# Optimization experiments

Hardware: AMD Instinct MI355X
Metric: run time of the kernel (lower is better)

Reference implementation:

```python
import jax, jax.numpy as jnp
import numpy as np

NGRID, NLAYER = 8192, 24
NPERIODS, NOBS, NC = 50, 4096, 200
SIGMA = 1.0
VREF = 3.0          # reference crustal Vs (km/s) for depth-sensitivity scale
RAYLEIGH_FACTOR = 0.92


def setup_inputs() -> dict:
    key = jax.random.key(0)
    k1, k2, k3 = jax.random.split(key, 3)
    # S-wave velocity model, 2.0-4.0 km/s, flattened as in log_prob(Vs_flat)
    Vs_flat = (2.0 + 2.0 * jax.random.uniform(k1, (NGRID, NLAYER))).reshape(-1).astype(jnp.float32)
    # Ray-path averaging matrix: nonnegative, rows sum to 1 (slowness average)
    A = jax.random.uniform(k2, (NOBS, NGRID), dtype=jnp.float32)
    A = A / A.sum(axis=1, keepdims=True)
    # Beamforming energy spectra per observation pair: (Nobs, Nperiods, Nc)
    energy = jax.random.uniform(k3, (NOBS, NPERIODS, NC), dtype=jnp.float32)
    # Monotone phase-velocity axis per observation: (Nobs, Nc)
    c_axis = jnp.zeros((NOBS, NC), jnp.float32) + jnp.linspace(1.5, 5.0, NC, dtype=jnp.float32)
    thick = jnp.full((NLAYER,), 2.0, jnp.float32)          # 2 km layers
    periods = jnp.linspace(1.0, 60.0, NPERIODS, dtype=jnp.float32)
    return {"Vs_flat": Vs_flat, "A": A, "energy": energy, "c_axis": c_axis,
            "thick": thick, "periods": periods}


def _dispersion_all_cells(Vs, thick, periods):
    # Differentiable surrogate for the batched surf96 forward across all grid cells.
    # Vs: (G, L), thick: (L,), periods: (P,)  ->  c_true: (G, P)
    z = jnp.cumsum(thick) - 0.5 * thick                      # layer-center depths (L,)
    depth_scale = VREF * periods / 3.0                       # ~ sensing depth per period (P,)
    w = jnp.exp(-z[None, :] / depth_scale[:, None]) * thick[None, :]  # (P, L)
    w = w / w.sum(axis=1, keepdims=True)
    return RAYLEIGH_FACTOR * jnp.einsum('pl,gl->gp', w, Vs)  # (G, P)


def reference(Vs_flat, A, energy, c_axis, thick, periods):
    Vs = Vs_flat.reshape(NGRID, NLAYER)
    c_true = _dispersion_all_cells(Vs, thick, periods)       # (Ngrid, Nperiods)
    # _apply_A: slowness averaging along ray paths
    s_pred = A @ (1.0 / c_true)                              # (Nobs, Nperiods)
    c_pred = 1.0 / s_pred
    # _interp1d_torch, vectorized over all (obs, period) pairs
    idx = jax.vmap(jnp.searchsorted)(c_axis, c_pred)         # (Nobs, Nperiods)
    idx = jnp.clip(idx, 1, NC - 1)
    c0 = jnp.take_along_axis(c_axis, idx - 1, axis=1)
    c1 = jnp.take_along_axis(c_axis, idx, axis=1)
    e0 = jnp.take_along_axis(energy, (idx - 1)[:, :, None], axis=2)[..., 0]
    e1 = jnp.take_along_axis(energy, idx[:, :, None], axis=2)[..., 0]
    w = (c_pred - c0) / (c1 - c0 + 1e-12)
    e_interp = e0 + w * (e1 - e0)
    e_max = energy.max(axis=-1)                              # (Nobs, Nperiods)
    log_like = -jnp.sum(e_max - e_interp) / (SIGMA ** 2)
    return log_like
```

## Files before the change

kernel.cpp:

```cpp
#include <hip/hip_runtime.h>

#define NGRID 8192
#define NLAYER 24
#define NPERIODS 50
#define NOBS 4096
#define NC 200
#define PP 64
#define NSPLIT 16
#define WPB 4
#define GC (NGRID / (NSPLIT * WPB))
#define KG 32
#define ASTR 36
#define NBINS 1024
#define OTILE 64
#define VREF 3.0f

__global__ __launch_bounds__(256) void k1_rpad(const float* __restrict__ Vs,
                                               const float* __restrict__ thick,
                                               const float* __restrict__ periods,
                                               float* __restrict__ r_pad,
                                               float* __restrict__ bins) {
    __shared__ float w_sh[NLAYER][NPERIODS];
    __shared__ float z_sh[NLAYER];
    int tid = threadIdx.x;
    if (blockIdx.x == 0) {
        for (int i = tid; i < NBINS; i += 256) bins[i] = 0.f;
    }
    if (tid < NLAYER) {
        float c = 0.f;
        for (int i = 0; i <= tid; ++i) c += thick[i];
        z_sh[tid] = c - 0.5f * thick[tid];
    }
    __syncthreads();
    if (tid < NPERIODS) {
        float ds = (VREF / 3.0f) * periods[tid];
        float tmp[NLAYER];
        float s = 0.f;
        #pragma unroll
        for (int l = 0; l < NLAYER; ++l) {
            float v = expf(-z_sh[l] / ds) * thick[l];
            tmp[l] = v; s += v;
        }
        float inv = 1.f / s;
        #pragma unroll
        for (int l = 0; l < NLAYER; ++l) w_sh[l][tid] = tmp[l] * inv;
    }
    __syncthreads();
    int idx = blockIdx.x * 256 + tid;
    int g = idx >> 6, p = idx & 63;
    float r = 0.f;
    if (p < NPERIODS) {
        const float4* vp = (const float4*)(Vs + (size_t)g * NLAYER);
        float s = 0.f;
        #pragma unroll
        for (int q = 0; q < NLAYER / 4; ++q) {
            float4 t = vp[q];
            s = fmaf(w_sh[4*q+0][p], t.x, s);
            s = fmaf(w_sh[4*q+1][p], t.y, s);
            s = fmaf(w_sh[4*q+2][p], t.z, s);
            s = fmaf(w_sh[4*q+3][p], t.w, s);
        }
        r = 1.0f / (0.92f * s);
    }
    r_pad[idx] = r;
}

__global__ __launch_bounds__(256) void k2_gemm(const float* __restrict__ A,
                                               const float* __restrict__ r_pad,
                                               float* __restrict__ partial) {
    __shared__ float lds[WPB * OTILE * ASTR];
    int tid  = threadIdx.x;
    int lane = tid & 63;
    int wv   = __builtin_amdgcn_readfirstlane(tid >> 6);
    int o_base = blockIdx.x * OTILE;
    int split  = blockIdx.y;
    float* Aw = lds + wv * (OTILE * ASTR);

    float acc[NPERIODS];
    #pragma unroll
    for (int p = 0; p < NPERIODS; ++p) acc[p] = 0.f;

    int g_wave = (split * WPB + wv) * GC;

    #pragma unroll 1
    for (int kt = 0; kt < GC / KG; ++kt) {
        int g0 = g_wave + kt * KG;
        #pragma unroll
        for (int s = 0; s < 8; ++s) {
            int f   = s * 64 + lane;
            int row = f >> 3;
            int c4  = (f & 7) * 4;
            float4 t = *(const float4*)(A + (size_t)(o_base + row) * NGRID + g0 + c4);
            *(float4*)(Aw + row * ASTR + c4) = t;
        }
        #pragma unroll 1
        for (int gg = 0; gg < KG; gg += 4) {
            float4 a4 = *(const float4*)(Aw + lane * ASTR + gg);
            const float* rr = r_pad + (size_t)(g0 + gg) * PP;
            #pragma unroll
            for (int j = 0; j < 4; ++j) {
                float aj = (j == 0) ? a4.x : (j == 1) ? a4.y : (j == 2) ? a4.z : a4.w;
                const float* rj = rr + j * PP;
                #pragma unroll
                for (int p = 0; p < NPERIODS; ++p) acc[p] = fmaf(aj, rj[p], acc[p]);
            }
        }
    }

    float* outp = partial + (size_t)split * (NOBS * NPERIODS) + (size_t)o_base * NPERIODS;
    #pragma unroll 1
    for (int h = 0; h < 4; ++h) {
        __syncthreads();
        float* rw = lds + wv * (OTILE * 17);
        #pragma unroll
        for (int q = 0; q < 16; ++q) {
            int p = h * 16 + q;
            rw[lane * 17 + q] = (p < NPERIODS) ? acc[p] : 0.f;
        }
        __syncthreads();
        for (int e = tid; e < OTILE * 16; e += 256) {
            int oo = e >> 4, q = e & 15;
            int p  = h * 16 + q;
            if (p < NPERIODS) {
                float v = 0.f;
                #pragma unroll
                for (int w2 = 0; w2 < WPB; ++w2) v += lds[w2 * (OTILE * 17) + oo * 17 + q];
                outp[oo * NPERIODS + p] = v;
            }
        }
    }
}

__global__ __launch_bounds__(256) void k2b_reduce(const float* __restrict__ partial,
                                                  float* __restrict__ cpred) {
    int idx = blockIdx.x * 256 + threadIdx.x;
    int o = idx >> 6, p = idx & 63;
    float v = 0.f;
    if (p < NPERIODS) {
        float s = 0.f;
        #pragma unroll
        for (int sp = 0; sp < NSPLIT; ++sp)
            s += partial[(size_t)sp * (NOBS * NPERIODS) + (size_t)o * NPERIODS + p];
        v = 1.0f / s;
    }
    cpred[idx] = v;
}

__global__ __launch_bounds__(256) void k3_main(const float* __restrict__ energy,
                                               const float* __restrict__ c_axis,
                                               const float* __restrict__ cpred,
                                               float* __restrict__ bins) {
    __shared__ float csh[NC];
    __shared__ float red[4];
    int tid  = threadIdx.x;
    int lane = tid & 63;
    int wv   = tid >> 6;
    int o    = blockIdx.x;

    if (tid < NC) csh[tid] = c_axis[(size_t)o * NC + tid];
    __syncthreads();

    bool act = lane < NC / 4;
    float4 ca = act ? *(const float4*)(csh + 4 * lane) : make_float4(9e30f, 9e30f, 9e30f, 9e30f);
    const float* ebase = energy + (size_t)o * NPERIODS * NC;
    float local = 0.f;

    for (int p0 = wv; p0 < NPERIODS; p0 += 8) {
        int p1 = p0 + 4;
        bool has1 = p1 < NPERIODS;
        int p1c = has1 ? p1 : p0;
        float cpA = cpred[(size_t)o * PP + p0];
        float cpB = cpred[(size_t)o * PP + p1c];
        const float* erA = ebase + (size_t)p0 * NC;
        const float* erB = ebase + (size_t)p1c * NC;
        float4 eA = act ? *(const float4*)(erA + 4 * lane) : make_float4(-1e30f, -1e30f, -1e30f, -1e30f);
        float4 eB = act ? *(const float4*)(erB + 4 * lane) : make_float4(-1e30f, -1e30f, -1e30f, -1e30f);

        int cntA = __popcll(__ballot(ca.x < cpA)) + __popcll(__ballot(ca.y < cpA))
                 + __popcll(__ballot(ca.z < cpA)) + __popcll(__ballot(ca.w < cpA));
        int cntB = __popcll(__ballot(ca.x < cpB)) + __popcll(__ballot(ca.y < cpB))
                 + __popcll(__ballot(ca.z < cpB)) + __popcll(__ballot(ca.w < cpB));

        float mA = fmaxf(fmaxf(eA.x, eA.y), fmaxf(eA.z, eA.w));
        float mB = fmaxf(fmaxf(eB.x, eB.y), fmaxf(eB.z, eB.w));
        #pragma unroll
        for (int m = 32; m; m >>= 1) {
            mA = fmaxf(mA, __shfl_xor(mA, m, 64));
            mB = fmaxf(mB, __shfl_xor(mB, m, 64));
        }

        int iA = cntA < 1 ? 1 : (cntA > NC - 1 ? NC - 1 : cntA);
        int iB = cntB < 1 ? 1 : (cntB > NC - 1 ? NC - 1 : cntB);

        int a0 = iA - 1, a1 = iA, b0 = iB - 1, b1 = iB;
        float sA0 = ((a0 & 3) == 0) ? eA.x : ((a0 & 3) == 1) ? eA.y : ((a0 & 3) == 2) ? eA.z : eA.w;
        float sA1 = ((a1 & 3) == 0) ? eA.x : ((a1 & 3) == 1) ? eA.y : ((a1 & 3) == 2) ? eA.z : eA.w;
        float sB0 = ((b0 & 3) == 0) ? eB.x : ((b0 & 3) == 1) ? eB.y : ((b0 & 3) == 2) ? eB.z : eB.w;
        float sB1 = ((b1 & 3) == 0) ? eB.x : ((b1 & 3) == 1) ? eB.y : ((b1 & 3) == 2) ? eB.z : eB.w;
        float e0A = __shfl(sA0, a0 >> 2, 64), e1A = __shfl(sA1, a1 >> 2, 64);
        float e0B = __shfl(sB0, b0 >> 2, 64), e1B = __shfl(sB1, b1 >> 2, 64);

        float c0A = csh[a0], c1A = csh[a1];
        float c0B = csh[b0], c1B = csh[b1];
        float wA = (cpA - c0A) / (c1A - c0A + 1e-12f);
        float wB = (cpB - c0B) / (c1B - c0B + 1e-12f);
        float eiA = fmaf(wA, e1A - e0A, e0A);
        float eiB = fmaf(wB, e1B - e0B, e0B);
        local += mA - eiA;
        local += has1 ? (mB - eiB) : 0.f;
    }
    if (lane == 0) red[wv] = local;
    __syncthreads();
    if (tid == 0)
        atomicAdd(&bins[blockIdx.x & (NBINS - 1)], red[0] + red[1] + red[2] + red[3]);
}

__global__ __launch_bounds__(256) void k4_final(const float* __restrict__ bins,
                                                float* __restrict__ out) {
    __shared__ float red[4];
    int tid = threadIdx.x;
    float s = 0.f;
    for (int i = tid; i < NBINS; i += 256) s += bins[i];
    #pragma unroll
    for (int m = 32; m; m >>= 1) s += __shfl_xor(s, m, 64);
    int lane = tid & 63, wv = tid >> 6;
    if (lane == 0) red[wv] = s;
    __syncthreads();
    if (tid == 0) out[0] = -(red[0] + red[1] + red[2] + red[3]);
}

extern "C" void kernel_launch(void* const* d_in, const int* in_sizes, int n_in,
                              void* d_out, int out_size, void* d_ws, size_t ws_size,
                              hipStream_t stream) {
    const float* Vs      = (const float*)d_in[0];
    const float* A       = (const float*)d_in[1];
    const float* energy  = (const float*)d_in[2];
    const float* c_axis  = (const float*)d_in[3];
    const float* thick   = (const float*)d_in[4];
    const float* periods = (const float*)d_in[5];
    float* out = (float*)d_out;

    float* ws      = (float*)d_ws;
    float* r_pad   = ws;
    float* partial = r_pad + (size_t)NGRID * PP;
    float* cpred   = partial + (size_t)NSPLIT * NOBS * NPERIODS;
    float* bins    = cpred + (size_t)NOBS * PP;

    hipLaunchKernelGGL(k1_rpad, dim3((NGRID * 64) / 256), dim3(256), 0, stream,
                       Vs, thick, periods, r_pad, bins);
    hipLaunchKernelGGL(k2_gemm, dim3(NOBS / OTILE, NSPLIT), dim3(256), 0, stream,
                       A, r_pad, partial);
    hipLaunchKernelGGL(k2b_reduce, dim3((NOBS * 64) / 256), dim3(256), 0, stream,
                       partial, cpred);
    hipLaunchKernelGGL(k3_main, dim3(NOBS), dim3(256), 0, stream,
                       energy, c_axis, cpred, bins);
    hipLaunchKernelGGL(k4_final, dim3(1), dim3(256), 0, stream, bins, out);
}
```

Before: 387.7 us.

## Fuse all stages into one cooperative persistent kernel with grid syncs

Replaces the five separate kernel launches with a single cooperative kernel that runs the dispersion precompute, GEMM, split reduction, interpolation and final sum as phases separated by grid.sync(). The grid is sized from occupancy and capped at 1024 blocks, with persistent loops over the work items of each phase. The aim is to remove per-launch overhead and the idle gaps between kernels. In exchange it adds grid-wide barrier cost, the register cap from launch_bounds(256,4) may cause spills in the 50-accumulator GEMM, and the old kernels stay as a fallback if the cooperative launch fails.

```diff
diff --git a/kernel.cpp b/kernel.cpp
--- a/kernel.cpp
+++ b/kernel.cpp
@@ -1,4 +1,7 @@
 #include <hip/hip_runtime.h>
+#include <hip/hip_cooperative_groups.h>
+
+namespace cg = cooperative_groups;
 
 #define NGRID 8192
 #define NLAYER 24
@@ -14,6 +17,228 @@
 #define NBINS 1024
 #define OTILE 64
 #define VREF 3.0f
+#define LDSF (WPB * OTILE * ASTR)
+
+__global__ __launch_bounds__(256, 4) void mega(
+        const float* __restrict__ Vs, const float* __restrict__ A,
+        const float* __restrict__ energy, const float* __restrict__ c_axis,
+        const float* __restrict__ thick, const float* __restrict__ periods,
+        float* __restrict__ r_pad, float* __restrict__ partial,
+        float* __restrict__ cpred, float* __restrict__ bins,
+        float* __restrict__ out) {
+    __shared__ float lds[LDSF];
+    cg::grid_group grid = cg::this_grid();
+    const int tid  = threadIdx.x;
+    const int lane = tid & 63;
+    const int bid  = blockIdx.x;
+    const int nblk = gridDim.x;
+
+    {
+        float* w_sh = lds;
+        float* z_sh = lds + NLAYER * NPERIODS;
+        for (int i = bid * 256 + tid; i < NBINS; i += nblk * 256) bins[i] = 0.f;
+        if (tid < NLAYER) {
+            float c = 0.f;
+            for (int i = 0; i <= tid; ++i) c += thick[i];
+            z_sh[tid] = c - 0.5f * thick[tid];
+        }
+        __syncthreads();
+        if (tid < NPERIODS) {
+            float ds = (VREF / 3.0f) * periods[tid];
+            float tmp[NLAYER];
+            float s = 0.f;
+            #pragma unroll
+            for (int l = 0; l < NLAYER; ++l) {
+                float v = expf(-z_sh[l] / ds) * thick[l];
+                tmp[l] = v; s += v;
+            }
+            float inv = 1.f / s;
+            #pragma unroll
+            for (int l = 0; l < NLAYER; ++l) w_sh[l * NPERIODS + tid] = tmp[l] * inv;
+        }
+        __syncthreads();
+        #pragma unroll 1
+        for (int vb = bid; vb < (NGRID * 64) / 256; vb += nblk) {
+            int idx = vb * 256 + tid;
+            int g = idx >> 6, p = idx & 63;
+            float r = 0.f;
+            if (p < NPERIODS) {
+                const float4* vp = (const float4*)(Vs + (size_t)g * NLAYER);
+                float s = 0.f;
+                #pragma unroll
+                for (int q = 0; q < NLAYER / 4; ++q) {
+                    float4 t = vp[q];
+                    s = fmaf(w_sh[(4*q+0) * NPERIODS + p], t.x, s);
+                    s = fmaf(w_sh[(4*q+1) * NPERIODS + p], t.y, s);
+                    s = fmaf(w_sh[(4*q+2) * NPERIODS + p], t.z, s);
+                    s = fmaf(w_sh[(4*q+3) * NPERIODS + p], t.w, s);
+                }
+                r = 1.0f / (0.92f * s);
+            }
+            r_pad[idx] = r;
+        }
+    }
+    grid.sync();
+
+    {
+        int wv = __builtin_amdgcn_readfirstlane(tid >> 6);
+        float* Aw = lds + wv * (OTILE * ASTR);
+        #pragma unroll 1
+        for (int t = bid; t < (NOBS / OTILE) * NSPLIT; t += nblk) {
+            __syncthreads();
+            int o_base = (t & (NOBS / OTILE - 1)) * OTILE;
+            int split  = t >> 6;
+            float acc[NPERIODS];
+            #pragma unroll
+            for (int p = 0; p < NPERIODS; ++p) acc[p] = 0.f;
+            int g_wave = (split * WPB + wv) * GC;
+
+            #pragma unroll 1
+            for (int kt = 0; kt < GC / KG; ++kt) {
+                int g0 = g_wave + kt * KG;
+                #pragma unroll
+                for (int s = 0; s < 8; ++s) {
+                    int f   = s * 64 + lane;
+                    int row = f >> 3;
+                    int c4  = (f & 7) * 4;
+                    float4 t4 = *(const float4*)(A + (size_t)(o_base + row) * NGRID + g0 + c4);
+                    *(float4*)(Aw + row * ASTR + c4) = t4;
+                }
+                #pragma unroll 1
+                for (int gg = 0; gg < KG; gg += 4) {
+                    float4 a4 = *(const float4*)(Aw + lane * ASTR + gg);
+                    const float* rr = r_pad + (size_t)(g0 + gg) * PP;
+                    #pragma unroll
+                    for (int j = 0; j < 4; ++j) {
+                        float aj = (j == 0) ? a4.x : (j == 1) ? a4.y : (j == 2) ? a4.z : a4.w;
+                        const float* rj = rr + j * PP;
+                        #pragma unroll
+                        for (int p = 0; p < NPERIODS; ++p) acc[p] = fmaf(aj, rj[p], acc[p]);
+                    }
+                }
+            }
+
+            float* outp = partial + (size_t)split * (NOBS * NPERIODS) + (size_t)o_base * NPERIODS;
+            #pragma unroll
+            for (int h = 0; h < 4; ++h) {
+                __syncthreads();
+                float* rw = lds + wv * (OTILE * 17);
+                #pragma unroll
+                for (int q = 0; q < 16; ++q) {
+                    int p = h * 16 + q;
+                    rw[lane * 17 + q] = (p < NPERIODS) ? acc[p] : 0.f;
+                }
+                __syncthreads();
+                for (int e = tid; e < OTILE * 16; e += 256) {
+                    int oo = e >> 4, q = e & 15;
+                    int p  = h * 16 + q;
+                    if (p < NPERIODS) {
+                        float v = 0.f;
+                        #pragma unroll
+                        for (int w2 = 0; w2 < WPB; ++w2) v += lds[w2 * (OTILE * 17) + oo * 17 + q];
+                        outp[oo * NPERIODS + p] = v;
+                    }
+                }
+            }
+        }
+    }
+    grid.sync();
+
+    #pragma unroll 1
+    for (int idx = bid * 256 + tid; idx < NOBS * 64; idx += nblk * 256) {
+        int o = idx >> 6, p = idx & 63;
+        float v = 0.f;
+        if (p < NPERIODS) {
+            float s = 0.f;
+            #pragma unroll
+            for (int sp = 0; sp < NSPLIT; ++sp)
+                s += partial[(size_t)sp * (NOBS * NPERIODS) + (size_t)o * NPERIODS + p];
+            v = 1.0f / s;
+        }
+        cpred[idx] = v;
+    }
+    grid.sync();
+
+    {
+        float* csh = lds;
+        float* red = lds + 256;
+        int wv = tid >> 6;
+        float blocksum = 0.f;
+        #pragma unroll 1
+        for (int o = bid; o < NOBS; o += nblk) {
+            __syncthreads();
+            if (tid < NC) csh[tid] = c_axis[(size_t)o * NC + tid];
+            __syncthreads();
+
+            bool act = lane < NC / 4;
+            float4 ca = act ? *(const float4*)(csh + 4 * lane) : make_float4(9e30f, 9e30f, 9e30f, 9e30f);
+            const float* ebase = energy + (size_t)o * NPERIODS * NC;
+            float local = 0.f;
+
+            for (int p0 = wv; p0 < NPERIODS; p0 += 8) {
+                int p1 = p0 + 4;
+                bool has1 = p1 < NPERIODS;
+                int p1c = has1 ? p1 : p0;
+                float cpA = cpred[(size_t)o * PP + p0];
+                float cpB = cpred[(size_t)o * PP + p1c];
+                const float* erA = ebase + (size_t)p0 * NC;
+                const float* erB = ebase + (size_t)p1c * NC;
+                float4 eA = act ? *(const float4*)(erA + 4 * lane) : make_float4(-1e30f, -1e30f, -1e30f, -1e30f);
+                float4 eB = act ? *(const float4*)(erB + 4 * lane) : make_float4(-1e30f, -1e30f, -1e30f, -1e30f);
+
+                int cntA = __popcll(__ballot(ca.x < cpA)) + __popcll(__ballot(ca.y < cpA))
+                         + __popcll(__ballot(ca.z < cpA)) + __popcll(__ballot(ca.w < cpA));
+                int cntB = __popcll(__ballot(ca.x < cpB)) + __popcll(__ballot(ca.y < cpB))
+                         + __popcll(__ballot(ca.z < cpB)) + __popcll(__ballot(ca.w < cpB));
+
+                float mA = fmaxf(fmaxf(eA.x, eA.y), fmaxf(eA.z, eA.w));
+                float mB = fmaxf(fmaxf(eB.x, eB.y), fmaxf(eB.z, eB.w));
+                #pragma unroll
+                for (int m = 32; m; m >>= 1) {
+                    mA = fmaxf(mA, __shfl_xor(mA, m, 64));
+                    mB = fmaxf(mB, __shfl_xor(mB, m, 64));
+                }
+
+                int iA = cntA < 1 ? 1 : (cntA > NC - 1 ? NC - 1 : cntA);
+                int iB = cntB < 1 ? 1 : (cntB > NC - 1 ? NC - 1 : cntB);
+
+                int a0 = iA - 1, a1 = iA, b0 = iB - 1, b1 = iB;
+                float sA0 = ((a0 & 3) == 0) ? eA.x : ((a0 & 3) == 1) ? eA.y : ((a0 & 3) == 2) ? eA.z : eA.w;
+                float sA1 = ((a1 & 3) == 0) ? eA.x : ((a1 & 3) == 1) ? eA.y : ((a1 & 3) == 2) ? eA.z : eA.w;
+                float sB0 = ((b0 & 3) == 0) ? eB.x : ((b0 & 3) == 1) ? eB.y : ((b0 & 3) == 2) ? eB.z : eB.w;
+                float sB1 = ((b1 & 3) == 0) ? eB.x : ((b1 & 3) == 1) ? eB.y : ((b1 & 3) == 2) ? eB.z : eB.w;
+                float e0A = __shfl(sA0, a0 >> 2, 64), e1A = __shfl(sA1, a1 >> 2, 64);
+                float e0B = __shfl(sB0, b0 >> 2, 64), e1B = __shfl(sB1, b1 >> 2, 64);
+
+                float c0A = csh[a0], c1A = csh[a1];
+                float c0B = csh[b0], c1B = csh[b1];
+                float wA = (cpA - c0A) / (c1A - c0A + 1e-12f);
+                float wB = (cpB - c0B) / (c1B - c0B + 1e-12f);
+                float eiA = fmaf(wA, e1A - e0A, e0A);
+                float eiB = fmaf(wB, e1B - e0B, e0B);
+                local += mA - eiA;
+                local += has1 ? (mB - eiB) : 0.f;
+            }
+            blocksum += local;
+        }
+        if (lane == 0) red[wv] = blocksum;
+        __syncthreads();
+        if (tid == 0)
+            atomicAdd(&bins[bid & (NBINS - 1)], red[0] + red[1] + red[2] + red[3]);
+    }
+    grid.sync();
+
+    if (bid == 0) {
+        float* red = lds + 256;
+        float s = 0.f;
+        for (int i = tid; i < NBINS; i += 256) s += bins[i];
+        #pragma unroll
+        for (int m = 32; m; m >>= 1) s += __shfl_xor(s, m, 64);
+        if (lane == 0) red[tid >> 6] = s;
+        __syncthreads();
+        if (tid == 0) out[0] = -(red[0] + red[1] + red[2] + red[3]);
+    }
+}
 
 __global__ __launch_bounds__(256) void k1_rpad(const float* __restrict__ Vs,
                                                const float* __restrict__ thick,
@@ -79,7 +304,6 @@
     float acc[NPERIODS];
     #pragma unroll
     for (int p = 0; p < NPERIODS; ++p) acc[p] = 0.f;
-
     int g_wave = (split * WPB + wv) * GC;
 
     #pragma unroll 1
@@ -106,9 +330,8 @@
             }
         }
     }
-
     float* outp = partial + (size_t)split * (NOBS * NPERIODS) + (size_t)o_base * NPERIODS;
-    #pragma unroll 1
+    #pragma unroll
     for (int h = 0; h < 4; ++h) {
         __syncthreads();
         float* rw = lds + wv * (OTILE * 17);
@@ -246,13 +469,29 @@
     float* cpred   = partial + (size_t)NSPLIT * NOBS * NPERIODS;
     float* bins    = cpred + (size_t)NOBS * PP;
 
-    hipLaunchKernelGGL(k1_rpad, dim3((NGRID * 64) / 256), dim3(256), 0, stream,
-                       Vs, thick, periods, r_pad, bins);
-    hipLaunchKernelGGL(k2_gemm, dim3(NOBS / OTILE, NSPLIT), dim3(256), 0, stream,
-                       A, r_pad, partial);
-    hipLaunchKernelGGL(k2b_reduce, dim3((NOBS * 64) / 256), dim3(256), 0, stream,
-                       partial, cpred);
-    hipLaunchKernelGGL(k3_main, dim3(NOBS), dim3(256), 0, stream,
-                       energy, c_axis, cpred, bins);
-    hipLaunchKernelGGL(k4_final, dim3(1), dim3(256), 0, stream, bins, out);
-}
+    static int nblk = 0;
+    if (nblk == 0) {
+        int nb = 0;
+        if (hipOccupancyMaxActiveBlocksPerMultiprocessor(&nb, (const void*)mega, 256, 0) != hipSuccess || nb < 1)
+            nb = 1;
+        long cap = (long)nb * 256;
+        nblk = (int)(cap < 1024 ? cap : 1024);
+    }
+
+    void* args[] = {(void*)&Vs, (void*)&A, (void*)&energy, (void*)&c_axis, (void*)&thick,
+                    (void*)&periods, (void*)&r_pad, (void*)&partial, (void*)&cpred,
+                    (void*)&bins, (void*)&out};
+    hipError_t err = hipLaunchCooperativeKernel((const void*)mega, dim3(nblk), dim3(256),
+                                                args, 0, stream);
+    if (err != hipSuccess) {
+        hipLaunchKernelGGL(k1_rpad, dim3((NGRID * 64) / 256), dim3(256), 0, stream,
+                           Vs, thick, periods, r_pad, bins);
+        hipLaunchKernelGGL(k2_gemm, dim3(NOBS / OTILE, NSPLIT), dim3(256), 0, stream,
+                           A, r_pad, partial);
+        hipLaunchKernelGGL(k2b_reduce, dim3((NOBS * 64) / 256), dim3(256), 0, stream,
+                           partial, cpred);
+        hipLaunchKernelGGL(k3_main, dim3(NOBS), dim3(256), 0, stream,
+                           energy, c_axis, cpred, bins);
+        hipLaunchKernelGGL(k4_final, dim3(1), dim3(256), 0, stream, bins, out);
+    }
+}
```

After: 816.6 us. 2.11x slower.

## Double per-lane GEMM rows and fuse split-reduce and final sum via last-block atomics

Applied to the files above, without the earlier changes.

The GEMM kernel now gives each lane two observation rows (tile of 128 rows, KG 16), so every loaded r_pad value feeds two FMAs and global reads of r_pad per FMA are halved. The separate split-reduction and final-sum kernels are removed. The last-arriving block, found with an atomic counter and thread fences, performs each reduction instead. Launch count and r_pad traffic drop, but register pressure rises with 100 accumulators, the grid shrinks to 512 blocks, and the counters add a serialized tail.

```diff
diff --git a/kernel.cpp b/kernel.cpp
--- a/kernel.cpp
+++ b/kernel.cpp
@@ -7,24 +7,26 @@
 #define NC 200
 #define PP 64
 #define NSPLIT 16
+#define SPLITG (NGRID / NSPLIT)
 #define WPB 4
-#define GC (NGRID / (NSPLIT * WPB))
-#define KG 32
-#define ASTR 36
+#define GC (SPLITG / WPB)
+#define KG 16
+#define ASTR 20
+#define DOT 128
 #define NBINS 1024
-#define OTILE 64
 #define VREF 3.0f
+#define K2LDSF (WPB * DOT * ASTR)
 
 __global__ __launch_bounds__(256) void k1_rpad(const float* __restrict__ Vs,
                                                const float* __restrict__ thick,
                                                const float* __restrict__ periods,
                                                float* __restrict__ r_pad,
-                                               float* __restrict__ bins) {
+                                               unsigned* __restrict__ zero_region) {
     __shared__ float w_sh[NLAYER][NPERIODS];
     __shared__ float z_sh[NLAYER];
     int tid = threadIdx.x;
     if (blockIdx.x == 0) {
-        for (int i = tid; i < NBINS; i += 256) bins[i] = 0.f;
+        for (int i = tid; i < NBINS + 32 + 1; i += 256) zero_region[i] = 0u;
     }
     if (tid < NLAYER) {
         float c = 0.f;
@@ -67,20 +69,23 @@
 
 __global__ __launch_bounds__(256) void k2_gemm(const float* __restrict__ A,
                                                const float* __restrict__ r_pad,
-                                               float* __restrict__ partial) {
-    __shared__ float lds[WPB * OTILE * ASTR];
+                                               float* __restrict__ partial,
+                                               float* __restrict__ cpred,
+                                               unsigned* __restrict__ cnt2) {
+    __shared__ float lds[K2LDSF];
+    __shared__ unsigned done_sh;
     int tid  = threadIdx.x;
     int lane = tid & 63;
     int wv   = __builtin_amdgcn_readfirstlane(tid >> 6);
-    int o_base = blockIdx.x * OTILE;
+    int o_base = blockIdx.x * DOT;
     int split  = blockIdx.y;
-    float* Aw = lds + wv * (OTILE * ASTR);
-
-    float acc[NPERIODS];
+    float* Aw = lds + wv * (DOT * ASTR);
+
+    float acc0[NPERIODS], acc1[NPERIODS];
     #pragma unroll
-    for (int p = 0; p < NPERIODS; ++p) acc[p] = 0.f;
-
-    int g_wave = (split * WPB + wv) * GC;
+    for (int p = 0; p < NPERIODS; ++p) { acc0[p] = 0.f; acc1[p] = 0.f; }
+
+    int g_wave = split * SPLITG + wv * GC;
 
     #pragma unroll 1
     for (int kt = 0; kt < GC / KG; ++kt) {
@@ -88,70 +93,84 @@
         #pragma unroll
         for (int s = 0; s < 8; ++s) {
             int f   = s * 64 + lane;
-            int row = f >> 3;
-            int c4  = (f & 7) * 4;
+            int row = f >> 2;
+            int c4  = (f & 3) * 4;
             float4 t = *(const float4*)(A + (size_t)(o_base + row) * NGRID + g0 + c4);
             *(float4*)(Aw + row * ASTR + c4) = t;
         }
         #pragma unroll 1
         for (int gg = 0; gg < KG; gg += 4) {
-            float4 a4 = *(const float4*)(Aw + lane * ASTR + gg);
+            float4 a0 = *(const float4*)(Aw + lane * ASTR + gg);
+            float4 a1 = *(const float4*)(Aw + (64 + lane) * ASTR + gg);
             const float* rr = r_pad + (size_t)(g0 + gg) * PP;
             #pragma unroll
             for (int j = 0; j < 4; ++j) {
-                float aj = (j == 0) ? a4.x : (j == 1) ? a4.y : (j == 2) ? a4.z : a4.w;
+                float aj0 = (j == 0) ? a0.x : (j == 1) ? a0.y : (j == 2) ? a0.z : a0.w;
+                float aj1 = (j == 0) ? a1.x : (j == 1) ? a1.y : (j == 2) ? a1.z : a1.w;
                 const float* rj = rr + j * PP;
                 #pragma unroll
-                for (int p = 0; p < NPERIODS; ++p) acc[p] = fmaf(aj, rj[p], acc[p]);
+                for (int p = 0; p < NPERIODS; ++p) {
+                    float rv = rj[p];
+                    acc0[p] = fmaf(aj0, rv, acc0[p]);
+                    acc1[p] = fmaf(aj1, rv, acc1[p]);
+                }
             }
         }
     }
 
     float* outp = partial + (size_t)split * (NOBS * NPERIODS) + (size_t)o_base * NPERIODS;
-    #pragma unroll 1
+    #pragma unroll
     for (int h = 0; h < 4; ++h) {
         __syncthreads();
-        float* rw = lds + wv * (OTILE * 17);
+        float* rw = lds + wv * (DOT * 17);
         #pragma unroll
         for (int q = 0; q < 16; ++q) {
             int p = h * 16 + q;
-            rw[lane * 17 + q] = (p < NPERIODS) ? acc[p] : 0.f;
+            rw[lane * 17 + q]        = (p < NPERIODS) ? acc0[p] : 0.f;
+            rw[(64 + lane) * 17 + q] = (p < NPERIODS) ? acc1[p] : 0.f;
         }
         __syncthreads();
-        for (int e = tid; e < OTILE * 16; e += 256) {
+        for (int e = tid; e < DOT * 16; e += 256) {
             int oo = e >> 4, q = e & 15;
             int p  = h * 16 + q;
             if (p < NPERIODS) {
                 float v = 0.f;
                 #pragma unroll
-                for (int w2 = 0; w2 < WPB; ++w2) v += lds[w2 * (OTILE * 17) + oo * 17 + q];
+                for (int w2 = 0; w2 < WPB; ++w2) v += lds[w2 * (DOT * 17) + oo * 17 + q];
                 outp[oo * NPERIODS + p] = v;
             }
         }
     }
-}
-
-__global__ __launch_bounds__(256) void k2b_reduce(const float* __restrict__ partial,
-                                                  float* __restrict__ cpred) {
-    int idx = blockIdx.x * 256 + threadIdx.x;
-    int o = idx >> 6, p = idx & 63;
-    float v = 0.f;
-    if (p < NPERIODS) {
-        float s = 0.f;
-        #pragma unroll
-        for (int sp = 0; sp < NSPLIT; ++sp)
-            s += partial[(size_t)sp * (NOBS * NPERIODS) + (size_t)o * NPERIODS + p];
-        v = 1.0f / s;
-    }
-    cpred[idx] = v;
+
+    __threadfence();
+    if (tid == 0) done_sh = atomicAdd(&cnt2[blockIdx.x], 1u);
+    __syncthreads();
+    if (done_sh == NSPLIT - 1) {
+        __threadfence();
+        for (int idx = tid; idx < DOT * 64; idx += 256) {
+            int oo = idx >> 6, p = idx & 63;
+            float v = 0.f;
+            if (p < NPERIODS) {
+                float s = 0.f;
+                #pragma unroll
+                for (int sp = 0; sp < NSPLIT; ++sp)
+                    s += partial[(size_t)sp * (NOBS * NPERIODS) + (size_t)(o_base + oo) * NPERIODS + p];
+                v = 1.0f / s;
+            }
+            cpred[(size_t)(o_base + oo) * PP + p] = v;
+        }
+    }
 }
 
 __global__ __launch_bounds__(256) void k3_main(const float* __restrict__ energy,
                                                const float* __restrict__ c_axis,
                                                const float* __restrict__ cpred,
-                                               float* __restrict__ bins) {
+                                               float* __restrict__ bins,
+                                               unsigned* __restrict__ cnt3,
+                                               float* __restrict__ out) {
     __shared__ float csh[NC];
     __shared__ float red[4];
+    __shared__ unsigned last_sh;
     int tid  = threadIdx.x;
     int lane = tid & 63;
     int wv   = tid >> 6;
@@ -213,20 +232,20 @@
     __syncthreads();
     if (tid == 0)
         atomicAdd(&bins[blockIdx.x & (NBINS - 1)], red[0] + red[1] + red[2] + red[3]);
-}
-
-__global__ __launch_bounds__(256) void k4_final(const float* __restrict__ bins,
-                                                float* __restrict__ out) {
-    __shared__ float red[4];
-    int tid = threadIdx.x;
-    float s = 0.f;
-    for (int i = tid; i < NBINS; i += 256) s += bins[i];
-    #pragma unroll
-    for (int m = 32; m; m >>= 1) s += __shfl_xor(s, m, 64);
-    int lane = tid & 63, wv = tid >> 6;
-    if (lane == 0) red[wv] = s;
-    __syncthreads();
-    if (tid == 0) out[0] = -(red[0] + red[1] + red[2] + red[3]);
+
+    __threadfence();
+    if (tid == 0) last_sh = atomicAdd(cnt3, 1u);
+    __syncthreads();
+    if (last_sh == gridDim.x - 1) {
+        __threadfence();
+        float s = 0.f;
+        for (int i = tid; i < NBINS; i += 256) s += bins[i];
+        #pragma unroll
+        for (int m = 32; m; m >>= 1) s += __shfl_xor(s, m, 64);
+        if (lane == 0) red[tid >> 6] = s;
+        __syncthreads();
+        if (tid == 0) out[0] = -(red[0] + red[1] + red[2] + red[3]);
+    }
 }
 
 extern "C" void kernel_launch(void* const* d_in, const int* in_sizes, int n_in,
@@ -245,14 +264,13 @@
     float* partial = r_pad + (size_t)NGRID * PP;
     float* cpred   = partial + (size_t)NSPLIT * NOBS * NPERIODS;
     float* bins    = cpred + (size_t)NOBS * PP;
+    unsigned* cnt2 = (unsigned*)(bins + NBINS);
+    unsigned* cnt3 = cnt2 + 32;
 
     hipLaunchKernelGGL(k1_rpad, dim3((NGRID * 64) / 256), dim3(256), 0, stream,
-                       Vs, thick, periods, r_pad, bins);
-    hipLaunchKernelGGL(k2_gemm, dim3(NOBS / OTILE, NSPLIT), dim3(256), 0, stream,
-                       A, r_pad, partial);
-    hipLaunchKernelGGL(k2b_reduce, dim3((NOBS * 64) / 256), dim3(256), 0, stream,
-                       partial, cpred);
+                       Vs, thick, periods, r_pad, (unsigned*)bins);
+    hipLaunchKernelGGL(k2_gemm, dim3(NOBS / DOT, NSPLIT), dim3(256), 0, stream,
+                       A, r_pad, partial, cpred, cnt2);
     hipLaunchKernelGGL(k3_main, dim3(NOBS), dim3(256), 0, stream,
-                       energy, c_axis, cpred, bins);
-    hipLaunchKernelGGL(k4_final, dim3(1), dim3(256), 0, stream, bins, out);
-}
+                       energy, c_axis, cpred, bins, cnt3, out);
+}
```

Result: slower. 845.8 us (+118.1%).
